# Kernel optimization log

Hardware: AMD Instinct MI355X
Metric: run time of the kernel (lower is better)

## Reference

```python
import jax, jax.numpy as jnp
import numpy as np

N_EX, N_KC, D, HID, NHEADS = 10000, 500, 128, 128, 2
B, S = 256, 500
ALPHA = 0.2
NEG = -9e15


def setup_inputs() -> dict:
    key = jax.random.key(0)
    ks = jax.random.split(key, 24)
    sc = 0.1
    inp = {
        "adj_exercise_kc": jax.random.randint(ks[0], (N_EX, N_KC), 0, 2, dtype=jnp.int32),
        "kc_data": jax.random.randint(ks[1], (B, S), 0, N_KC).astype(jnp.int64),
        "exercise_data": jax.random.randint(ks[2], (B, S), 0, N_EX + 1).astype(jnp.int64),
        "exercise_respond_data": jax.random.randint(ks[3], (B, S), 0, 2 * N_EX + 1).astype(jnp.int64),
        "target": jax.random.randint(ks[4], (B * (S - 1), 1), 0, 2).astype(jnp.float32),
        # learned parameters
        "ex_embed": jax.random.normal(ks[5], (N_EX, D)) * sc,
        "kc_embed": jax.random.normal(ks[6], (N_KC, D)) * sc,
        "W1": jax.random.normal(ks[7], (NHEADS, D, D)) * sc,        # per-head shared proj
        "a_att": jax.random.normal(ks[8], (NHEADS, 2 * D, 1)) * sc,  # attention vector
        "E": jax.random.normal(ks[9], (NHEADS, D, D)) * sc,
        "rd_w": jax.random.normal(ks[10], (NHEADS, D, 2 * D)) * sc,  # reduceDim (mode 3)
        "rd_b": jnp.zeros((NHEADS, D)),
        "w_ih": jax.random.normal(ks[11], (4 * HID, 2 * D)) * sc,
        "w_hh": jax.random.normal(ks[12], (4 * HID, HID)) * sc,
        "b_ih": jnp.zeros((4 * HID,)),
        "b_hh": jnp.zeros((4 * HID,)),
        "fc1_w": jax.random.normal(ks[13], (HID, D + HID)) * sc,
        "fc1_b": jnp.zeros((HID,)),
        "fc2_w": jax.random.normal(ks[14], (1, HID)) * sc,
        "fc2_b": jnp.zeros((1,)),
    }
    return inp


def _gat_head(ex_h, kc_h, adj, W1h, ah, Eh, rdw, rdb):
    # mode == 3 GAT head. a_input @ a decomposes: e[i,j] = LReLU(exWh[i].a1 + kcWh[j].a2)
    kc_Wh = kc_h @ W1h                                   # [Nkc, D]
    ex_Wh = ex_h @ W1h                                   # [Nex, D]
    e = jax.nn.leaky_relu(ex_Wh @ ah[:D] + (kc_Wh @ ah[D:]).T, ALPHA)  # [Nex, Nkc]
    att = jax.nn.softmax(jnp.where(adj > 0, e, NEG), axis=1)
    new_kc = att @ kc_Wh                                 # [Nex, D]
    ex_Eh = ex_h @ Eh
    emb = jnp.concatenate([new_kc, new_kc * ex_Eh], axis=1) @ rdw.T + rdb
    return jax.nn.elu(emb)                               # [Nex, D]


def _lstm(x, w_ih, w_hh, b_ih, b_hh):
    # single-layer torch LSTM, gate order i,f,g,o
    b = x.shape[0]
    xg = jnp.einsum('bsi,gi->sbg', x, w_ih) + b_ih + b_hh  # [S,B,4H]

    def step(carry, xt):
        h, c = carry
        g = xt + h @ w_hh.T
        i, f, gg, o = jnp.split(g, 4, axis=-1)
        c = jax.nn.sigmoid(f) * c + jax.nn.sigmoid(i) * jnp.tanh(gg)
        h = jax.nn.sigmoid(o) * jnp.tanh(c)
        return (h, c), h

    init = (jnp.zeros((b, HID), x.dtype), jnp.zeros((b, HID), x.dtype))
    _, hs = jax.lax.scan(step, init, xg)
    return jnp.swapaxes(hs, 0, 1)                        # [B,S,H]


def _forward(adj, exercise_data, respond_data, target,
             ex_embed, kc_embed, W1, a_att, E, rd_w, rd_b,
             w_ih, w_hh, b_ih, b_hh, fc1_w, fc1_b, fc2_w, fc2_b):
    heads = jax.vmap(_gat_head, in_axes=(None, None, None, 0, 0, 0, 0, 0))(
        ex_embed, kc_embed, adj, W1, a_att, E, rd_w, rd_b)   # [NH, Nex, D]
    # torch: cat(dim=1).view(Nex, D, NH).mean(2) -> interleaved reshape of the concat
    cat = jnp.swapaxes(heads, 0, 1).reshape(N_EX, NHEADS * D)
    exercise_embedding = cat.reshape(N_EX, D, NHEADS).mean(-1)  # [Nex, D]

    emb0 = jnp.concatenate([jnp.zeros((1, D), exercise_embedding.dtype), exercise_embedding], 0)
    assess = emb0[exercise_data]                          # [B,S,D]

    zeros = jnp.zeros_like(exercise_embedding)
    resp_emb = jnp.concatenate([
        jnp.concatenate([zeros, exercise_embedding], -1),
        jnp.concatenate([exercise_embedding, zeros], -1)], 0)  # [2Nex, 2D]
    resp0 = jnp.concatenate([jnp.zeros((1, 2 * D), resp_emb.dtype), resp_emb], 0)
    lstm_input = resp0[respond_data]                      # [B,S,2D]

    learn = _lstm(lstm_input, w_ih, w_hh, b_ih, b_hh)[:, :S - 1, :]  # [B,S-1,H]
    assess = assess[:, 1:, :]                             # [B,S-1,D]

    y = jax.nn.relu(jnp.concatenate([learn, assess], -1) @ fc1_w.T + fc1_b)
    pred = (y @ fc2_w.T + fc2_b).reshape(-1)              # [B*(S-1)]
    t = target.reshape(-1)                                # all targets >= 0 => mask all-true
    # BCE with logits, mean reduction
    loss = jnp.mean(jnp.maximum(pred, 0) - pred * t + jnp.log1p(jnp.exp(-jnp.abs(pred))))
    return loss, jax.nn.sigmoid(pred), t


def reference(adj_exercise_kc, kc_data, exercise_data, exercise_respond_data, target,
              ex_embed, kc_embed, W1, a_att, E, rd_w, rd_b,
              w_ih, w_hh, b_ih, b_hh, fc1_w, fc1_b, fc2_w, fc2_b):
    del kc_data  # unused by the original forward body
    return _forward(adj_exercise_kc, exercise_data, exercise_respond_data, target,
                    ex_embed, kc_embed, W1, a_att, E, rd_w, rd_b,
                    w_ih, w_hh, b_ih, b_hh, fc1_w, fc1_b, fc2_w, fc2_b)
```

## Files before the change

kernel.cpp:

```cpp
#include <hip/hip_runtime.h>
#include <math.h>

#define N_EX 10000
#define N_KC 500
#define D 128
#define HID 128
#define BB 256
#define SS 500
#define NROWS 127744

typedef float vf4 __attribute__((ext_vector_type(4)));
typedef _Float16 hf2 __attribute__((ext_vector_type(2)));

__device__ __forceinline__ float sigm(float x) { return 1.f / (1.f + __expf(-x)); }
__device__ __forceinline__ float tanh_fast(float x) { return 1.f - 2.f / (1.f + __expf(2.f * x)); }

__device__ __forceinline__ hf2 u2h(unsigned v) { union { unsigned u; hf2 h; } x; x.u = v; return x.h; }

__device__ __forceinline__ float quad_sum(float x) {
    int a = __builtin_amdgcn_update_dpp(0, __float_as_int(x), 0xB1, 0xF, 0xF, true);
    x += __int_as_float(a);
    int b = __builtin_amdgcn_update_dpp(0, __float_as_int(x), 0x4E, 0xF, 0xF, true);
    x += __int_as_float(b);
    return x;
}

__global__ void k_precomp(const float* rd_w, const float* w_ih, const float* fc1_w,
                          const float* b_ih, const float* b_hh, const float* W1, const float* a_att,
                          const float* w_hh,
                          float* rd_wT, float* w_ihT0, float* w_ihT1,
                          float* fc1_AT, float* fc1_BT, float* gbias4, float* v1,
                          unsigned short* wlstm16, float* projC) {
    int idx = blockIdx.x * blockDim.x + threadIdx.x;
    int stride = gridDim.x * blockDim.x;
    const int N1 = 2 * 256 * 128;
    const int N2 = 128 * 512;
    const int N3 = 128 * 512;
    const int N4 = 128 * 128;
    const int N5 = 128 * 128;
    const int N6 = 512;
    const int N7 = 256;
    const int N8 = 65536;
    int total = N1 + N2 + N3 + N4 + N5 + N6 + N7 + N8;
    for (int tt = idx; tt < total; tt += stride) {
        int u = tt;
        if (u < N1) {
            int h = u / (256 * 128); int rem = u % (256 * 128); int c = rem / 128; int dd = rem % 128;
            rd_wT[u] = rd_w[h * 128 * 256 + dd * 256 + c];
        } else if ((u -= N1) < N2) {
            int k = u / 512, g = u % 512; w_ihT0[u] = w_ih[g * 256 + k];
        } else if ((u -= N2) < N3) {
            int k = u / 512, g = u % 512; w_ihT1[u] = w_ih[g * 256 + 128 + k];
        } else if ((u -= N3) < N4) {
            int k = u / 128, j = u % 128; fc1_AT[u] = fc1_w[j * 256 + k];
        } else if ((u -= N4) < N5) {
            int k = u / 128, j = u % 128; fc1_BT[u] = fc1_w[j * 256 + 128 + k];
        } else if ((u -= N5) < N6) {
            int uu = u >> 2, g = u & 3;
            float v = b_ih[g * 128 + uu] + b_hh[g * 128 + uu];
            gbias4[u] = v;
            projC[u] = v;
        } else if ((u -= N6) < N7) {
            int h = u / 128, k = u % 128;
            const float* wr = W1 + h * 16384 + k * 128;
            const float* av = a_att + h * 256;
            float acc = 0.f;
            for (int d = 0; d < 128; ++d) acc += wr[d] * av[d];
            v1[u] = acc;
        } else {
            u -= N7;
            int x = u & 7;
            int t = (u >> 3) & 511;
            int i = u >> 12;
            int g = i >> 2, j = i & 3;
            int uu = t >> 2, q = t & 3;
            float val = w_hh[(g * 128 + uu) * 128 + q * 32 + j * 8 + x];
            ((_Float16*)wlstm16)[u] = (_Float16)val;
        }
    }
}

__global__ void k_kc(const float* kc_embed, const float* W1, const float* a_att,
                     float* kcWhT, float* s_kc) {
    int j = blockIdx.x, h = blockIdx.y, d = threadIdx.x;
    __shared__ float row[128];
    __shared__ float red[128];
    row[d] = kc_embed[j * 128 + d];
    __syncthreads();
    const float* w = W1 + h * 16384;
    float acc = 0.f;
    for (int k = 0; k < 128; ++k) acc += row[k] * w[k * 128 + d];
    kcWhT[((size_t)(h * 128 + d)) * 500 + j] = acc;
    red[d] = acc * a_att[h * 256 + 128 + d];
    __syncthreads();
    for (int s = 64; s > 0; s >>= 1) { if (d < s) red[d] += red[d + s]; __syncthreads(); }
    if (d == 0) s_kc[h * 500 + j] = red[0];
}

__global__ void k_sex(const float* ex_embed, const float* v1, float* s_ex) {
    int t = blockIdx.x * blockDim.x + threadIdx.x;
    if (t >= 2 * N_EX) return;
    int h = t / N_EX, i = t % N_EX;
    const float4* e4 = (const float4*)(ex_embed + (size_t)i * 128);
    const float4* v4 = (const float4*)(v1 + h * 128);
    float acc = 0.f;
    for (int k = 0; k < 32; ++k) {
        float4 a = e4[k], b = v4[k];
        acc += a.x * b.x + a.y * b.y + a.z * b.z + a.w * b.w;
    }
    s_ex[h * N_EX + i] = acc;
}

__global__ __launch_bounds__(256) void k_attnk(const int* adj, const float* s_ex, const float* s_kc,
                                               const float* kcWhT, float* new_kc) {
    int i0 = blockIdx.x * 8, h = blockIdx.y, t = threadIdx.x;
    __shared__ vf4 at4[1500];
    __shared__ float skc_l[500];
    float* at = (float*)at4;
    for (int j = t; j < 500; j += 256) skc_l[j] = s_kc[h * 500 + j];
    __syncthreads();
    {
        int lg = t >> 5, lane = t & 31;
        int i = i0 + lg;
        float sex = s_ex[h * N_EX + i];
        const int* arow = adj + (size_t)i * 500;
        float lmax = -INFINITY;
        for (int j = lane; j < 500; j += 32) {
            float e = sex + skc_l[j];
            e = (e >= 0.f) ? e : 0.2f * e;
            e = (arow[j] > 0) ? e : -INFINITY;
            at[j * 12 + lg] = e;
            lmax = fmaxf(lmax, e);
        }
#pragma unroll
        for (int m = 16; m > 0; m >>= 1) lmax = fmaxf(lmax, __shfl_xor(lmax, m));
        float lsum = 0.f;
        for (int j = lane; j < 500; j += 32) {
            float w = __expf(at[j * 12 + lg] - lmax);
            at[j * 12 + lg] = w;
            lsum += w;
        }
#pragma unroll
        for (int m = 16; m > 0; m >>= 1) lsum += __shfl_xor(lsum, m);
        float inv = 1.f / lsum;
        for (int j = lane; j < 500; j += 32) at[j * 12 + lg] *= inv;
    }
    __syncthreads();
    int d = t & 127, half = t >> 7;
    const float* kcwd = kcWhT + ((size_t)(h * 128 + d)) * 500;
    vf4 acc = {0.f, 0.f, 0.f, 0.f};
    for (int j4 = 0; j4 < 125; ++j4) {
        vf4 w = *(const vf4*)(kcwd + j4 * 4);
        vf4 a0 = *(const vf4*)(at + (j4 * 4 + 0) * 12 + half * 4);
        vf4 a1 = *(const vf4*)(at + (j4 * 4 + 1) * 12 + half * 4);
        vf4 a2 = *(const vf4*)(at + (j4 * 4 + 2) * 12 + half * 4);
        vf4 a3 = *(const vf4*)(at + (j4 * 4 + 3) * 12 + half * 4);
        acc += a0 * w.x + a1 * w.y + a2 * w.z + a3 * w.w;
    }
    new_kc[((size_t)h * N_EX + i0 + half * 4 + 0) * 128 + d] = acc.x;
    new_kc[((size_t)h * N_EX + i0 + half * 4 + 1) * 128 + d] = acc.y;
    new_kc[((size_t)h * N_EX + i0 + half * 4 + 2) * 128 + d] = acc.z;
    new_kc[((size_t)h * N_EX + i0 + half * 4 + 3) * 128 + d] = acc.w;
}

__global__ __launch_bounds__(256) void k_gat2(const float* new_kc, const float* ex_embed,
                                              const float* E, const float* rd_wT,
                                              const float* rd_b, float* H) {
    int i0 = blockIdx.x * 8, h = blockIdx.y, t = threadIdx.x;
    int d = t & 127, half = t >> 7;
    __shared__ vf4 exrT4[256], nkT4[256], prT4[256];
    float* exrT = (float*)exrT4;
    float* nkT  = (float*)nkT4;
    float* prT  = (float*)prT4;
    for (int idx = t; idx < 8 * 128; idx += 256) {
        int r = idx >> 7, k = idx & 127;
        exrT[k * 8 + r] = ex_embed[(size_t)i0 * 128 + idx];
        nkT[k * 8 + r]  = new_kc[((size_t)h * N_EX + i0) * 128 + idx];
    }
    __syncthreads();
    const float* Eh = E + h * 16384;
    vf4 acc2 = {0.f, 0.f, 0.f, 0.f};
    for (int k = 0; k < 128; ++k) {
        float ev = Eh[k * 128 + d];
        vf4 ex4 = *(const vf4*)(exrT + k * 8 + half * 4);
        acc2 += ex4 * ev;
    }
    {
        vf4 nk4 = *(const vf4*)(nkT + d * 8 + half * 4);
        vf4 pr4 = nk4 * acc2;
        *(vf4*)(prT + d * 8 + half * 4) = pr4;
    }
    __syncthreads();
    const float* rt = rd_wT + h * 256 * 128;
    vf4 acc3 = {0.f, 0.f, 0.f, 0.f};
    for (int c = 0; c < 128; ++c) {
        float w = rt[c * 128 + d];
        vf4 nk4 = *(const vf4*)(nkT + c * 8 + half * 4);
        acc3 += nk4 * w;
    }
    for (int c = 0; c < 128; ++c) {
        float w = rt[(128 + c) * 128 + d];
        vf4 pr4 = *(const vf4*)(prT + c * 8 + half * 4);
        acc3 += pr4 * w;
    }
    float rb = rd_b[h * 128 + d];
#pragma unroll
    for (int r = 0; r < 4; ++r) {
        float v = ((r == 0) ? acc3.x : (r == 1) ? acc3.y : (r == 2) ? acc3.z : acc3.w) + rb;
        v = (v > 0.f) ? v : expm1f(v);
        H[((size_t)h * N_EX + i0 + half * 4 + r) * 128 + d] = v;
    }
}

__global__ void k_merge(const float* H, float* emb_e) {
    int idx = blockIdx.x * blockDim.x + threadIdx.x;
    if (idx >= N_EX * 128) return;
    int i = idx >> 7, d = idx & 127;
    int hs = d >> 6;
    int c0 = (2 * d) & 127, c1 = (2 * d + 1) & 127;
    const float* row = H + ((size_t)hs * N_EX + i) * 128;
    emb_e[idx] = 0.5f * (row[c0] + row[c1]);
}

__global__ __launch_bounds__(512) void k_proj(const float* emb_e, const float* w_ihT0,
                                              const float* w_ihT1, const float* fc1_BT,
                                              const float* gbias4,
                                              float* projC, float* assessP) {
    int i0 = blockIdx.x * 16, g = threadIdx.x;
    int gate = g >> 7, uu = g & 127;
    int oidx = uu * 4 + gate;
    float gbl = gbias4[oidx];
    __shared__ float er[16 * 128];
    for (int idx = g; idx < 16 * 128; idx += 512) er[idx] = emb_e[(size_t)i0 * 128 + idx];
    __syncthreads();
    float a0[16], a1[16];
#pragma unroll
    for (int r = 0; r < 16; ++r) { a0[r] = 0.f; a1[r] = 0.f; }
    for (int k = 0; k < 128; ++k) {
        float w0 = w_ihT0[k * 512 + g], w1 = w_ihT1[k * 512 + g];
#pragma unroll
        for (int r = 0; r < 16; ++r) { float e = er[r * 128 + k]; a0[r] += e * w0; a1[r] += e * w1; }
    }
    for (int r = 0; r < 16; ++r) {
        projC[((size_t)(1 + i0 + r)) * 512 + oidx]        = a1[r] + gbl;
        projC[((size_t)(1 + N_EX + i0 + r)) * 512 + oidx] = a0[r] + gbl;
    }
    if (g < 128) {
        float b[16];
#pragma unroll
        for (int r = 0; r < 16; ++r) b[r] = 0.f;
        for (int k = 0; k < 128; ++k) {
            float w = fc1_BT[k * 128 + g];
#pragma unroll
            for (int r = 0; r < 16; ++r) b[r] += er[r * 128 + k] * w;
        }
        for (int r = 0; r < 16; ++r) assessP[((size_t)i0 + r) * 128 + g] = b[r];
    }
}

__global__ __launch_bounds__(512, 2) void k_lstm(const uint4* __restrict__ w16,
                                                 const float* __restrict__ projC,
                                                 const int* __restrict__ respond,
                                                 unsigned short* __restrict__ learn16) {
    int b = blockIdx.x, t = threadIdx.x;
    int u = t >> 2, q = t & 3;
    __shared__ uint4 hbuf4[2][18];
    __shared__ int rrow[500];
    uint4 w[16];
#pragma unroll
    for (int i = 0; i < 16; ++i) w[i] = w16[i * 512 + t];
    for (int s = t; s < 500; s += 512) rrow[s] = respond[b * 500 + s];
    if (t < 36) { uint4 z = {0u, 0u, 0u, 0u}; ((uint4*)hbuf4)[t] = z; }
    float c = 0.f;
    __syncthreads();
    vf4 xg_n = ((const vf4*)(projC + (size_t)rrow[0] * 512))[u];
    for (int s = 0; s < 500; ++s) {
        int par = s & 1;
        vf4 xg = xg_n;
        if (s < 499) xg_n = ((const vf4*)(projC + (size_t)rrow[s + 1] * 512))[u];
        const uint4* hsegp = (const uint4*)((const unsigned short*)hbuf4[par] + q * 32);
        uint4 h4[4];
#pragma unroll
        for (int j = 0; j < 4; ++j) h4[j] = hsegp[j];
        float p0 = 0.f, p1 = 0.f, p2 = 0.f, p3 = 0.f;
#pragma unroll
        for (int j = 0; j < 4; ++j) {
            hf2 ha = u2h(h4[j].x), hb = u2h(h4[j].y), hc = u2h(h4[j].z), hd = u2h(h4[j].w);
            uint4 w0 = w[j], w1 = w[4 + j], w2 = w[8 + j], w3 = w[12 + j];
            p0 = __builtin_amdgcn_fdot2(u2h(w0.x), ha, p0, false);
            p0 = __builtin_amdgcn_fdot2(u2h(w0.y), hb, p0, false);
            p0 = __builtin_amdgcn_fdot2(u2h(w0.z), hc, p0, false);
            p0 = __builtin_amdgcn_fdot2(u2h(w0.w), hd, p0, false);
            p1 = __builtin_amdgcn_fdot2(u2h(w1.x), ha, p1, false);
            p1 = __builtin_amdgcn_fdot2(u2h(w1.y), hb, p1, false);
            p1 = __builtin_amdgcn_fdot2(u2h(w1.z), hc, p1, false);
            p1 = __builtin_amdgcn_fdot2(u2h(w1.w), hd, p1, false);
            p2 = __builtin_amdgcn_fdot2(u2h(w2.x), ha, p2, false);
            p2 = __builtin_amdgcn_fdot2(u2h(w2.y), hb, p2, false);
            p2 = __builtin_amdgcn_fdot2(u2h(w2.z), hc, p2, false);
            p2 = __builtin_amdgcn_fdot2(u2h(w2.w), hd, p2, false);
            p3 = __builtin_amdgcn_fdot2(u2h(w3.x), ha, p3, false);
            p3 = __builtin_amdgcn_fdot2(u2h(w3.y), hb, p3, false);
            p3 = __builtin_amdgcn_fdot2(u2h(w3.z), hc, p3, false);
            p3 = __builtin_amdgcn_fdot2(u2h(w3.w), hd, p3, false);
        }
        float gi = quad_sum(p0) + xg.x;
        float gf = quad_sum(p1) + xg.y;
        float gG = quad_sum(p2) + xg.z;
        float go = quad_sum(p3) + xg.w;
        float ii = sigm(gi), ff = sigm(gf), tg = tanh_fast(gG), oo = sigm(go);
        c = ff * c + ii * tg;
        float hh = oo * tanh_fast(c);
        if (q == 0) {
            union { unsigned short us; _Float16 hf; } cv; cv.hf = (_Float16)hh;
            ((unsigned short*)hbuf4[par ^ 1])[u] = cv.us;
            if (s < 499) learn16[((size_t)b * 499 + s) * 128 + u] = cv.us;
        }
        __syncthreads();
    }
}

__global__ __launch_bounds__(256) void k_mlp(const unsigned short* __restrict__ learn16,
                                             const float* __restrict__ assessP,
                                             const float* __restrict__ fc1_AT,
                                             const float* __restrict__ fc1_b,
                                             const float* __restrict__ fc2_w,
                                             const float* __restrict__ fc2_b,
                                             const int* __restrict__ exercise_data,
                                             const float* __restrict__ target,
                                             float* __restrict__ out,
                                             float* __restrict__ loss_accum) {
    int tile = blockIdx.x;
    int t = threadIdx.x;
    int jg = t & 31, rg = t >> 5;
    __shared__ float A_lds[64 * 128];
    __shared__ float x_lds[64 * 64];
    __shared__ float red[8];
    float4 acc[8];
#pragma unroll
    for (int r = 0; r < 8; ++r) acc[r] = make_float4(0.f, 0.f, 0.f, 0.f);
    int row0 = tile * 64;
    for (int kc = 0; kc < 2; ++kc) {
        for (int idx = t; idx < 64 * 128; idx += 256) A_lds[idx] = fc1_AT[kc * 64 * 128 + idx];
        for (int idx = t; idx < 64 * 32; idx += 256) {
            int r = idx >> 5, k2 = idx & 31;
            unsigned pv = *(const unsigned*)(learn16 + ((size_t)row0 + r) * 128 + kc * 64 + k2 * 2);
            hf2 hp = u2h(pv);
            x_lds[(r << 6) + k2 * 2]     = (float)hp.x;
            x_lds[(r << 6) + k2 * 2 + 1] = (float)hp.y;
        }
        __syncthreads();
        const float4* A4 = (const float4*)A_lds;
        const float4* x4 = (const float4*)x_lds;
#pragma unroll 4
        for (int k4 = 0; k4 < 16; ++k4) {
            float4 av[4];
#pragma unroll
            for (int kk = 0; kk < 4; ++kk) av[kk] = A4[(k4 * 4 + kk) * 32 + jg];
#pragma unroll
            for (int r = 0; r < 8; ++r) {
                float4 xv = x4[(rg * 8 + r) * 16 + k4];
                acc[r].x += xv.x * av[0].x + xv.y * av[1].x + xv.z * av[2].x + xv.w * av[3].x;
                acc[r].y += xv.x * av[0].y + xv.y * av[1].y + xv.z * av[2].y + xv.w * av[3].y;
                acc[r].z += xv.x * av[0].z + xv.y * av[1].z + xv.z * av[2].z + xv.w * av[3].z;
                acc[r].w += xv.x * av[0].w + xv.y * av[1].w + xv.z * av[2].w + xv.w * av[3].w;
            }
        }
        __syncthreads();
    }
    int j = jg * 4;
    float4 b1 = *(const float4*)(fc1_b + j);
    float4 f2 = *(const float4*)(fc2_w + j);
    float fb2 = fc2_b[0];
    float lloss = 0.f;
#pragma unroll
    for (int r = 0; r < 8; ++r) {
        int n = row0 + rg * 8 + r;
        int b = n / 499;
        int sidx = n - b * 499;
        int e = exercise_data[b * 500 + sidx + 1];
        float4 aP = make_float4(0.f, 0.f, 0.f, 0.f);
        if (e > 0) aP = *(const float4*)(assessP + (size_t)(e - 1) * 128 + j);
        float y0 = acc[r].x + aP.x + b1.x; y0 = y0 > 0.f ? y0 : 0.f;
        float y1 = acc[r].y + aP.y + b1.y; y1 = y1 > 0.f ? y1 : 0.f;
        float y2 = acc[r].z + aP.z + b1.z; y2 = y2 > 0.f ? y2 : 0.f;
        float y3 = acc[r].w + aP.w + b1.w; y3 = y3 > 0.f ? y3 : 0.f;
        float s = y0 * f2.x + y1 * f2.y + y2 * f2.z + y3 * f2.w;
#pragma unroll
        for (int m = 16; m > 0; m >>= 1) s += __shfl_xor(s, m, 32);
        if (jg == 0) {
            float p = s + fb2;
            float tg = target[n];
            out[1 + n] = 1.f / (1.f + expf(-p));
            float ab = fabsf(p);
            lloss += fmaxf(p, 0.f) - p * tg + log1pf(expf(-ab));
            out[1 + NROWS + n] = tg;
        }
    }
    if (jg == 0) red[rg] = lloss;
    __syncthreads();
    if (t == 0) {
        float sum = 0.f;
#pragma unroll
        for (int g = 0; g < 8; ++g) sum += red[g];
        atomicAdd(loss_accum, sum);
    }
}

__global__ void k_final(const float* loss_accum, float* out) {
    out[0] = loss_accum[0] * (1.f / (float)NROWS);
}

extern "C" void kernel_launch(void* const* d_in, const int* in_sizes, int n_in,
                              void* d_out, int out_size, void* d_ws, size_t ws_size,
                              hipStream_t stream) {
    const int* adj            = (const int*)d_in[0];
    const int* exercise_data  = (const int*)d_in[2];
    const int* respond        = (const int*)d_in[3];
    const float* target       = (const float*)d_in[4];
    const float* ex_embed     = (const float*)d_in[5];
    const float* kc_embed     = (const float*)d_in[6];
    const float* W1           = (const float*)d_in[7];
    const float* a_att        = (const float*)d_in[8];
    const float* E            = (const float*)d_in[9];
    const float* rd_w         = (const float*)d_in[10];
    const float* rd_b         = (const float*)d_in[11];
    const float* w_ih         = (const float*)d_in[12];
    const float* w_hh         = (const float*)d_in[13];
    const float* b_ih         = (const float*)d_in[14];
    const float* b_hh         = (const float*)d_in[15];
    const float* fc1_w        = (const float*)d_in[16];
    const float* fc1_b        = (const float*)d_in[17];
    const float* fc2_w        = (const float*)d_in[18];
    const float* fc2_b        = (const float*)d_in[19];
    float* out = (float*)d_out;

    float* ws = (float*)d_ws;
    size_t off = 0;
    auto alloc = [&](size_t n) { float* p = ws + off; off += (n + 3) & ~(size_t)3; return p; };
    float* kcWhT   = alloc(2 * 128 * 500);
    float* s_kc    = alloc(1000);
    float* v1      = alloc(256);
    float* s_ex    = alloc(2 * N_EX);
    float* H       = alloc((size_t)2 * N_EX * 128);
    float* emb_e   = alloc((size_t)N_EX * 128);
    float* rd_wT   = alloc(2 * 256 * 128);
    float* w_ihT0  = alloc(128 * 512);
    float* w_ihT1  = alloc(128 * 512);
    float* fc1_AT  = alloc(128 * 128);
    float* fc1_BT  = alloc(128 * 128);
    float* gbias4  = alloc(512);
    float* wlstm   = alloc(32768);
    float* new_kc  = alloc((size_t)2 * N_EX * 128);
    float* projC   = alloc((size_t)(2 * N_EX + 1) * 512);
    float* assessP = alloc((size_t)N_EX * 128);
    float* learn16 = alloc((size_t)BB * 499 * 64);
    float* loss_accum = alloc(4);

    k_precomp<<<256, 256, 0, stream>>>(rd_w, w_ih, fc1_w, b_ih, b_hh, W1, a_att, w_hh,
                                       rd_wT, w_ihT0, w_ihT1, fc1_AT, fc1_BT, gbias4, v1,
                                       (unsigned short*)wlstm, projC);
    k_kc<<<dim3(500, 2), 128, 0, stream>>>(kc_embed, W1, a_att, kcWhT, s_kc);
    k_sex<<<79, 256, 0, stream>>>(ex_embed, v1, s_ex);
    k_attnk<<<dim3(N_EX / 8, 2), 256, 0, stream>>>(adj, s_ex, s_kc, kcWhT, new_kc);
    k_gat2<<<dim3(N_EX / 8, 2), 256, 0, stream>>>(new_kc, ex_embed, E, rd_wT, rd_b, H);
    k_merge<<<(N_EX * 128) / 256, 256, 0, stream>>>(H, emb_e);
    k_proj<<<N_EX / 16, 512, 0, stream>>>(emb_e, w_ihT0, w_ihT1, fc1_BT, gbias4, projC, assessP);
    hipMemsetAsync(loss_accum, 0, sizeof(float), stream);
    k_lstm<<<BB, 512, 0, stream>>>((const uint4*)wlstm, projC, respond,
                                   (unsigned short*)learn16);
    k_mlp<<<NROWS / 64, 256, 0, stream>>>((const unsigned short*)learn16, assessP, fc1_AT,
                                          fc1_b, fc2_w, fc2_b,
                                          exercise_data, target, out, loss_accum);
    k_final<<<1, 1, 0, stream>>>(loss_accum, out);
}
```

Before: 803.2 us.

## Fuse both GAT heads per block and merge head averaging into gat kernel

The attention kernel now handles both heads in one block, so each adjacency row is read once instead of twice. The GAT output kernel computes both heads and writes the merged, averaged embedding directly, which removes the intermediate H buffer and the separate merge kernel. projC gate columns change from interleaved to gate-major order, and the LSTM now loads four scalars per step instead of one vf4. The fused kernels issue fewer blocks, use more shared memory per block and do more serial work each, which may lower occupancy.

```diff
diff --git a/kernel.cpp b/kernel.cpp
--- a/kernel.cpp
+++ b/kernel.cpp
@@ -29,7 +29,7 @@
                           const float* b_ih, const float* b_hh, const float* W1, const float* a_att,
                           const float* w_hh,
                           float* rd_wT, float* w_ihT0, float* w_ihT1,
-                          float* fc1_AT, float* fc1_BT, float* gbias4, float* v1,
+                          float* fc1_AT, float* fc1_BT, float* v1,
                           unsigned short* wlstm16, float* projC) {
     int idx = blockIdx.x * blockDim.x + threadIdx.x;
     int stride = gridDim.x * blockDim.x;
@@ -56,10 +56,7 @@
         } else if ((u -= N4) < N5) {
             int k = u / 128, j = u % 128; fc1_BT[u] = fc1_w[j * 256 + 128 + k];
         } else if ((u -= N5) < N6) {
-            int uu = u >> 2, g = u & 3;
-            float v = b_ih[g * 128 + uu] + b_hh[g * 128 + uu];
-            gbias4[u] = v;
-            projC[u] = v;
+            projC[u] = b_ih[u] + b_hh[u];
         } else if ((u -= N6) < N7) {
             int h = u / 128, k = u % 128;
             const float* wr = W1 + h * 16384 + k * 128;
@@ -113,123 +110,142 @@
 
 __global__ __launch_bounds__(256) void k_attnk(const int* adj, const float* s_ex, const float* s_kc,
                                                const float* kcWhT, float* new_kc) {
-    int i0 = blockIdx.x * 8, h = blockIdx.y, t = threadIdx.x;
-    __shared__ vf4 at4[1500];
-    __shared__ float skc_l[500];
-    float* at = (float*)at4;
-    for (int j = t; j < 500; j += 256) skc_l[j] = s_kc[h * 500 + j];
+    int i0 = blockIdx.x * 8, t = threadIdx.x;
+    __shared__ vf4 at4[2][1500];
+    __shared__ float skc_l[2][500];
+    float* at0 = (float*)at4[0];
+    float* at1 = (float*)at4[1];
+    for (int j = t; j < 1000; j += 256) ((float*)skc_l)[j] = s_kc[j];
     __syncthreads();
     {
         int lg = t >> 5, lane = t & 31;
         int i = i0 + lg;
-        float sex = s_ex[h * N_EX + i];
+        float sex0 = s_ex[i];
+        float sex1 = s_ex[N_EX + i];
         const int* arow = adj + (size_t)i * 500;
-        float lmax = -INFINITY;
+        float lmax0 = -INFINITY, lmax1 = -INFINITY;
         for (int j = lane; j < 500; j += 32) {
-            float e = sex + skc_l[j];
-            e = (e >= 0.f) ? e : 0.2f * e;
-            e = (arow[j] > 0) ? e : -INFINITY;
-            at[j * 12 + lg] = e;
-            lmax = fmaxf(lmax, e);
-        }
-#pragma unroll
-        for (int m = 16; m > 0; m >>= 1) lmax = fmaxf(lmax, __shfl_xor(lmax, m));
-        float lsum = 0.f;
+            bool m = arow[j] > 0;
+            float e0 = sex0 + skc_l[0][j];
+            e0 = (e0 >= 0.f) ? e0 : 0.2f * e0;
+            e0 = m ? e0 : -INFINITY;
+            float e1 = sex1 + skc_l[1][j];
+            e1 = (e1 >= 0.f) ? e1 : 0.2f * e1;
+            e1 = m ? e1 : -INFINITY;
+            at0[j * 12 + lg] = e0;
+            at1[j * 12 + lg] = e1;
+            lmax0 = fmaxf(lmax0, e0);
+            lmax1 = fmaxf(lmax1, e1);
+        }
+#pragma unroll
+        for (int m = 16; m > 0; m >>= 1) {
+            lmax0 = fmaxf(lmax0, __shfl_xor(lmax0, m));
+            lmax1 = fmaxf(lmax1, __shfl_xor(lmax1, m));
+        }
+        float lsum0 = 0.f, lsum1 = 0.f;
         for (int j = lane; j < 500; j += 32) {
-            float w = __expf(at[j * 12 + lg] - lmax);
-            at[j * 12 + lg] = w;
-            lsum += w;
-        }
-#pragma unroll
-        for (int m = 16; m > 0; m >>= 1) lsum += __shfl_xor(lsum, m);
-        float inv = 1.f / lsum;
-        for (int j = lane; j < 500; j += 32) at[j * 12 + lg] *= inv;
+            float w0 = __expf(at0[j * 12 + lg] - lmax0);
+            float w1 = __expf(at1[j * 12 + lg] - lmax1);
+            at0[j * 12 + lg] = w0;
+            at1[j * 12 + lg] = w1;
+            lsum0 += w0; lsum1 += w1;
+        }
+#pragma unroll
+        for (int m = 16; m > 0; m >>= 1) {
+            lsum0 += __shfl_xor(lsum0, m);
+            lsum1 += __shfl_xor(lsum1, m);
+        }
+        float inv0 = 1.f / lsum0, inv1 = 1.f / lsum1;
+        for (int j = lane; j < 500; j += 32) {
+            at0[j * 12 + lg] *= inv0;
+            at1[j * 12 + lg] *= inv1;
+        }
     }
     __syncthreads();
     int d = t & 127, half = t >> 7;
-    const float* kcwd = kcWhT + ((size_t)(h * 128 + d)) * 500;
-    vf4 acc = {0.f, 0.f, 0.f, 0.f};
-    for (int j4 = 0; j4 < 125; ++j4) {
-        vf4 w = *(const vf4*)(kcwd + j4 * 4);
-        vf4 a0 = *(const vf4*)(at + (j4 * 4 + 0) * 12 + half * 4);
-        vf4 a1 = *(const vf4*)(at + (j4 * 4 + 1) * 12 + half * 4);
-        vf4 a2 = *(const vf4*)(at + (j4 * 4 + 2) * 12 + half * 4);
-        vf4 a3 = *(const vf4*)(at + (j4 * 4 + 3) * 12 + half * 4);
-        acc += a0 * w.x + a1 * w.y + a2 * w.z + a3 * w.w;
-    }
-    new_kc[((size_t)h * N_EX + i0 + half * 4 + 0) * 128 + d] = acc.x;
-    new_kc[((size_t)h * N_EX + i0 + half * 4 + 1) * 128 + d] = acc.y;
-    new_kc[((size_t)h * N_EX + i0 + half * 4 + 2) * 128 + d] = acc.z;
-    new_kc[((size_t)h * N_EX + i0 + half * 4 + 3) * 128 + d] = acc.w;
-}
-
-__global__ __launch_bounds__(256) void k_gat2(const float* new_kc, const float* ex_embed,
-                                              const float* E, const float* rd_wT,
-                                              const float* rd_b, float* H) {
-    int i0 = blockIdx.x * 8, h = blockIdx.y, t = threadIdx.x;
+    for (int h = 0; h < 2; ++h) {
+        const float* at = (h == 0) ? at0 : at1;
+        const float* kcwd = kcWhT + ((size_t)(h * 128 + d)) * 500;
+        vf4 acc = {0.f, 0.f, 0.f, 0.f};
+        for (int j4 = 0; j4 < 125; ++j4) {
+            vf4 w = *(const vf4*)(kcwd + j4 * 4);
+            vf4 a0 = *(const vf4*)(at + (j4 * 4 + 0) * 12 + half * 4);
+            vf4 a1 = *(const vf4*)(at + (j4 * 4 + 1) * 12 + half * 4);
+            vf4 a2 = *(const vf4*)(at + (j4 * 4 + 2) * 12 + half * 4);
+            vf4 a3 = *(const vf4*)(at + (j4 * 4 + 3) * 12 + half * 4);
+            acc += a0 * w.x + a1 * w.y + a2 * w.z + a3 * w.w;
+        }
+        new_kc[((size_t)h * N_EX + i0 + half * 4 + 0) * 128 + d] = acc.x;
+        new_kc[((size_t)h * N_EX + i0 + half * 4 + 1) * 128 + d] = acc.y;
+        new_kc[((size_t)h * N_EX + i0 + half * 4 + 2) * 128 + d] = acc.z;
+        new_kc[((size_t)h * N_EX + i0 + half * 4 + 3) * 128 + d] = acc.w;
+    }
+}
+
+__global__ __launch_bounds__(256) void k_gat2m(const float* new_kc, const float* ex_embed,
+                                               const float* E, const float* rd_wT,
+                                               const float* rd_b, float* emb_e) {
+    int i0 = blockIdx.x * 8, t = threadIdx.x;
     int d = t & 127, half = t >> 7;
-    __shared__ vf4 exrT4[256], nkT4[256], prT4[256];
-    float* exrT = (float*)exrT4;
-    float* nkT  = (float*)nkT4;
-    float* prT  = (float*)prT4;
+    __shared__ float exrT[128 * 8];
+    __shared__ float nkT[2][128 * 8];
+    __shared__ float prT[128 * 8];
+    __shared__ float Hl[2][8 * 128];
     for (int idx = t; idx < 8 * 128; idx += 256) {
         int r = idx >> 7, k = idx & 127;
-        exrT[k * 8 + r] = ex_embed[(size_t)i0 * 128 + idx];
-        nkT[k * 8 + r]  = new_kc[((size_t)h * N_EX + i0) * 128 + idx];
-    }
-    __syncthreads();
-    const float* Eh = E + h * 16384;
-    vf4 acc2 = {0.f, 0.f, 0.f, 0.f};
-    for (int k = 0; k < 128; ++k) {
-        float ev = Eh[k * 128 + d];
-        vf4 ex4 = *(const vf4*)(exrT + k * 8 + half * 4);
-        acc2 += ex4 * ev;
-    }
-    {
-        vf4 nk4 = *(const vf4*)(nkT + d * 8 + half * 4);
-        vf4 pr4 = nk4 * acc2;
-        *(vf4*)(prT + d * 8 + half * 4) = pr4;
-    }
-    __syncthreads();
-    const float* rt = rd_wT + h * 256 * 128;
-    vf4 acc3 = {0.f, 0.f, 0.f, 0.f};
-    for (int c = 0; c < 128; ++c) {
-        float w = rt[c * 128 + d];
-        vf4 nk4 = *(const vf4*)(nkT + c * 8 + half * 4);
-        acc3 += nk4 * w;
-    }
-    for (int c = 0; c < 128; ++c) {
-        float w = rt[(128 + c) * 128 + d];
-        vf4 pr4 = *(const vf4*)(prT + c * 8 + half * 4);
-        acc3 += pr4 * w;
-    }
-    float rb = rd_b[h * 128 + d];
-#pragma unroll
-    for (int r = 0; r < 4; ++r) {
-        float v = ((r == 0) ? acc3.x : (r == 1) ? acc3.y : (r == 2) ? acc3.z : acc3.w) + rb;
-        v = (v > 0.f) ? v : expm1f(v);
-        H[((size_t)h * N_EX + i0 + half * 4 + r) * 128 + d] = v;
-    }
-}
-
-__global__ void k_merge(const float* H, float* emb_e) {
-    int idx = blockIdx.x * blockDim.x + threadIdx.x;
-    if (idx >= N_EX * 128) return;
-    int i = idx >> 7, d = idx & 127;
-    int hs = d >> 6;
-    int c0 = (2 * d) & 127, c1 = (2 * d + 1) & 127;
-    const float* row = H + ((size_t)hs * N_EX + i) * 128;
-    emb_e[idx] = 0.5f * (row[c0] + row[c1]);
+        exrT[k * 8 + r]   = ex_embed[(size_t)i0 * 128 + idx];
+        nkT[0][k * 8 + r] = new_kc[((size_t)i0) * 128 + idx];
+        nkT[1][k * 8 + r] = new_kc[((size_t)N_EX + i0) * 128 + idx];
+    }
+    __syncthreads();
+    for (int h = 0; h < 2; ++h) {
+        const float* Eh = E + h * 16384;
+        const float* rt = rd_wT + h * 256 * 128;
+        float rb = rd_b[h * 128 + d];
+        vf4 acc2 = {0.f, 0.f, 0.f, 0.f};
+        for (int k = 0; k < 128; ++k) {
+            float ev = Eh[k * 128 + d];
+            vf4 ex4 = *(const vf4*)(exrT + k * 8 + half * 4);
+            acc2 += ex4 * ev;
+        }
+        {
+            vf4 nk4 = *(const vf4*)(nkT[h] + d * 8 + half * 4);
+            *(vf4*)(prT + d * 8 + half * 4) = nk4 * acc2;
+        }
+        __syncthreads();
+        vf4 acc3 = {0.f, 0.f, 0.f, 0.f};
+        for (int c = 0; c < 128; ++c) {
+            float w = rt[c * 128 + d];
+            vf4 nk4 = *(const vf4*)(nkT[h] + c * 8 + half * 4);
+            acc3 += nk4 * w;
+        }
+        for (int c = 0; c < 128; ++c) {
+            float w = rt[(128 + c) * 128 + d];
+            vf4 pr4 = *(const vf4*)(prT + c * 8 + half * 4);
+            acc3 += pr4 * w;
+        }
+#pragma unroll
+        for (int r = 0; r < 4; ++r) {
+            float v = ((r == 0) ? acc3.x : (r == 1) ? acc3.y : (r == 2) ? acc3.z : acc3.w) + rb;
+            v = (v > 0.f) ? v : expm1f(v);
+            Hl[h][(half * 4 + r) * 128 + d] = v;
+        }
+        __syncthreads();
+    }
+    for (int idx = t; idx < 8 * 128; idx += 256) {
+        int r = idx >> 7, dd = idx & 127;
+        int hs = dd >> 6;
+        int c0 = (2 * dd) & 127, c1 = (2 * dd + 1) & 127;
+        emb_e[((size_t)i0 + r) * 128 + dd] = 0.5f * (Hl[hs][r * 128 + c0] + Hl[hs][r * 128 + c1]);
+    }
 }
 
 __global__ __launch_bounds__(512) void k_proj(const float* emb_e, const float* w_ihT0,
                                               const float* w_ihT1, const float* fc1_BT,
-                                              const float* gbias4,
+                                              const float* b_ih, const float* b_hh,
                                               float* projC, float* assessP) {
     int i0 = blockIdx.x * 16, g = threadIdx.x;
-    int gate = g >> 7, uu = g & 127;
-    int oidx = uu * 4 + gate;
-    float gbl = gbias4[oidx];
+    float gbl = b_ih[g] + b_hh[g];
     __shared__ float er[16 * 128];
     for (int idx = g; idx < 16 * 128; idx += 512) er[idx] = emb_e[(size_t)i0 * 128 + idx];
     __syncthreads();
@@ -242,8 +258,8 @@
         for (int r = 0; r < 16; ++r) { float e = er[r * 128 + k]; a0[r] += e * w0; a1[r] += e * w1; }
     }
     for (int r = 0; r < 16; ++r) {
-        projC[((size_t)(1 + i0 + r)) * 512 + oidx]        = a1[r] + gbl;
-        projC[((size_t)(1 + N_EX + i0 + r)) * 512 + oidx] = a0[r] + gbl;
+        projC[((size_t)(1 + i0 + r)) * 512 + g]        = a1[r] + gbl;
+        projC[((size_t)(1 + N_EX + i0 + r)) * 512 + g] = a0[r] + gbl;
     }
     if (g < 128) {
         float b[16];
@@ -273,11 +289,15 @@
     if (t < 36) { uint4 z = {0u, 0u, 0u, 0u}; ((uint4*)hbuf4)[t] = z; }
     float c = 0.f;
     __syncthreads();
-    vf4 xg_n = ((const vf4*)(projC + (size_t)rrow[0] * 512))[u];
+    const float* pc0 = projC + (size_t)rrow[0] * 512;
+    float x0n = pc0[u], x1n = pc0[128 + u], x2n = pc0[256 + u], x3n = pc0[384 + u];
     for (int s = 0; s < 500; ++s) {
         int par = s & 1;
-        vf4 xg = xg_n;
-        if (s < 499) xg_n = ((const vf4*)(projC + (size_t)rrow[s + 1] * 512))[u];
+        float x0 = x0n, x1 = x1n, x2 = x2n, x3 = x3n;
+        if (s < 499) {
+            const float* pc = projC + (size_t)rrow[s + 1] * 512;
+            x0n = pc[u]; x1n = pc[128 + u]; x2n = pc[256 + u]; x3n = pc[384 + u];
+        }
         const uint4* hsegp = (const uint4*)((const unsigned short*)hbuf4[par] + q * 32);
         uint4 h4[4];
 #pragma unroll
@@ -304,10 +324,10 @@
             p3 = __builtin_amdgcn_fdot2(u2h(w3.z), hc, p3, false);
             p3 = __builtin_amdgcn_fdot2(u2h(w3.w), hd, p3, false);
         }
-        float gi = quad_sum(p0) + xg.x;
-        float gf = quad_sum(p1) + xg.y;
-        float gG = quad_sum(p2) + xg.z;
-        float go = quad_sum(p3) + xg.w;
+        float gi = quad_sum(p0) + x0;
+        float gf = quad_sum(p1) + x1;
+        float gG = quad_sum(p2) + x2;
+        float go = quad_sum(p3) + x3;
         float ii = sigm(gi), ff = sigm(gf), tg = tanh_fast(gG), oo = sigm(go);
         c = ff * c + ii * tg;
         float hh = oo * tanh_fast(c);
@@ -442,14 +462,12 @@
     float* s_kc    = alloc(1000);
     float* v1      = alloc(256);
     float* s_ex    = alloc(2 * N_EX);
-    float* H       = alloc((size_t)2 * N_EX * 128);
     float* emb_e   = alloc((size_t)N_EX * 128);
     float* rd_wT   = alloc(2 * 256 * 128);
     float* w_ihT0  = alloc(128 * 512);
     float* w_ihT1  = alloc(128 * 512);
     float* fc1_AT  = alloc(128 * 128);
     float* fc1_BT  = alloc(128 * 128);
-    float* gbias4  = alloc(512);
     float* wlstm   = alloc(32768);
     float* new_kc  = alloc((size_t)2 * N_EX * 128);
     float* projC   = alloc((size_t)(2 * N_EX + 1) * 512);
@@ -458,14 +476,14 @@
     float* loss_accum = alloc(4);
 
     k_precomp<<<256, 256, 0, stream>>>(rd_w, w_ih, fc1_w, b_ih, b_hh, W1, a_att, w_hh,
-                                       rd_wT, w_ihT0, w_ihT1, fc1_AT, fc1_BT, gbias4, v1,
+                                       rd_wT, w_ihT0, w_ihT1, fc1_AT, fc1_BT, v1,
                                        (unsigned short*)wlstm, projC);
     k_kc<<<dim3(500, 2), 128, 0, stream>>>(kc_embed, W1, a_att, kcWhT, s_kc);
     k_sex<<<79, 256, 0, stream>>>(ex_embed, v1, s_ex);
-    k_attnk<<<dim3(N_EX / 8, 2), 256, 0, stream>>>(adj, s_ex, s_kc, kcWhT, new_kc);
-    k_gat2<<<dim3(N_EX / 8, 2), 256, 0, stream>>>(new_kc, ex_embed, E, rd_wT, rd_b, H);
-    k_merge<<<(N_EX * 128) / 256, 256, 0, stream>>>(H, emb_e);
-    k_proj<<<N_EX / 16, 512, 0, stream>>>(emb_e, w_ihT0, w_ihT1, fc1_BT, gbias4, projC, assessP);
+    k_attnk<<<N_EX / 8, 256, 0, stream>>>(adj, s_ex, s_kc, kcWhT, new_kc);
+    k_gat2m<<<N_EX / 8, 256, 0, stream>>>(new_kc, ex_embed, E, rd_wT, rd_b, emb_e);
+    k_proj<<<N_EX / 16, 512, 0, stream>>>(emb_e, w_ihT0, w_ihT1, fc1_BT, b_ih, b_hh,
+                                          projC, assessP);
     hipMemsetAsync(loss_accum, 0, sizeof(float), stream);
     k_lstm<<<BB, 512, 0, stream>>>((const uint4*)wlstm, projC, respond,
                                    (unsigned short*)learn16);
```

After: 800.7 us. About the same (-0.3%).
